# Kernel optimization log

Measured on AMD Instinct MI355X. Metric: run time of the kernel, lower is better.

The kernel has to match this reference:

```python
import jax, jax.numpy as jnp
import numpy as np

FP8 = jnp.float8_e4m3fn
FP8_MAX = 448.0  # float8_e4m3fn max finite value used by the module


def setup_inputs() -> dict:
    key = jax.random.key(0)
    k1, k2, k3 = jax.random.split(key, 3)
    x = jax.random.normal(k1, (4096, 4096), dtype=jnp.float32)          # [tokens, in_features]
    weight = jax.random.normal(k2, (16384, 4096), dtype=jnp.float32) * 0.02  # [out, in] fp32 master weight
    bias = jax.random.normal(k3, (16384,), dtype=jnp.float32) * 0.01
    return {"x": x, "weight": weight, "bias": bias}


def reference(x, weight, bias):
    # quantize_weight: per-tensor scale from fp32 weight, cast to fp8 (saturating)
    w_scale = FP8_MAX / (jnp.max(jnp.abs(weight)) + 1e-6)
    w_fp8 = (weight * w_scale).astype(FP8)
    # quantize_activation: per-tensor dynamic scale
    x_abs_max = jnp.max(jnp.abs(x)) + 1e-6
    x_scale = FP8_MAX / x_abs_max
    x_fp8 = (x * x_scale).astype(FP8)
    # upcast fp8 -> fp32 matmul, then descale + bias (same as torch module)
    out = jnp.matmul(x_fp8.astype(jnp.float32), w_fp8.astype(jnp.float32).T)
    out = out / (x_scale * w_scale)
    out = out + bias
    return out.astype(FP8)
```

## Files before the change

kernel.cpp:

```cpp
#include <hip/hip_runtime.h>
#include <math.h>
#include <stdint.h>

#define TOK  4096
#define KIN  4096
#define NOUT 16384

#define BM 128
#define BN 128
#define BK 64

#define FBM 64
#define FBN 64
#define FBK 32
#define FLDP (FBK + 2)

typedef int int32x4  __attribute__((ext_vector_type(4)));
typedef int int32x16 __attribute__((ext_vector_type(16)));

__global__ void init_ws_kernel(unsigned int* hdr) {
  if (threadIdx.x < 2) hdr[threadIdx.x] = 0u;
}

__global__ void absmax_kernel(const float4* __restrict__ src, int n4,
                              unsigned int* __restrict__ dst) {
  float m = 0.0f;
  for (int i = blockIdx.x * blockDim.x + threadIdx.x; i < n4;
       i += gridDim.x * blockDim.x) {
    float4 v = src[i];
    m = fmaxf(m, fmaxf(fmaxf(fabsf(v.x), fabsf(v.y)),
                       fmaxf(fabsf(v.z), fabsf(v.w))));
  }
#pragma unroll
  for (int off = 32; off > 0; off >>= 1) m = fmaxf(m, __shfl_down(m, off, 64));
  __shared__ float sm[4];
  if ((threadIdx.x & 63) == 0) sm[threadIdx.x >> 6] = m;
  __syncthreads();
  if (threadIdx.x == 0) {
    m = fmaxf(fmaxf(sm[0], sm[1]), fmaxf(sm[2], sm[3]));
    atomicMax(dst, __float_as_uint(m));
  }
}

__device__ __forceinline__ float scale_f32(unsigned int maxbits) {
  return __fdiv_rn(448.0f, __fadd_rn(__uint_as_float(maxbits), 1e-6f));
}

__device__ __forceinline__ unsigned char enc_fp8_f32(float v) {
  unsigned char s = (v < 0.0f) ? 0x80 : 0x00;
  float a = fabsf(v);
  if (a == 0.0f) return s;
  int e2;
  (void)frexpf(a, &e2);
  int p = e2 - 4;
  if (p < -9) p = -9;
  int n = (int)rintf(ldexpf(a, -p));
  if (n == 16) { n = 8; p += 1; }
  int E, mm;
  if (n >= 8) { E = p + 10; mm = n - 8; }
  else        { E = 0;      mm = n;     }
  return (unsigned char)(s | (E << 3) | mm);
}

__device__ __forceinline__ double out_value(double v) {
  if (v == 0.0) return 0.0;
  double a = fabs(v);
  int e2;
  (void)frexp(a, &e2);
  int p = e2 - 4;
  if (p < -9) p = -9;
  double t = ldexp(a, -p);
  double r;
  if (p <= -2) {
    r = ldexp(floor(t) + 0.5, p);
  } else {
    int n = (int)rint(t);
    if (n == 16) { n = 8; p += 1; }
    r = ldexp((double)n, p);
  }
  return (v < 0.0) ? -r : r;
}

__global__ void encode_kernel(const float* __restrict__ src, int n,
                              const unsigned int* __restrict__ maxbits,
                              unsigned char* __restrict__ codes) {
  const float scale = scale_f32(*maxbits);
  for (int i = blockIdx.x * blockDim.x + threadIdx.x; i < n;
       i += gridDim.x * blockDim.x) {
    codes[i] = enc_fp8_f32(__fmul_rn(src[i], scale));
  }
}

__global__ void encode_digits_kernel(const float4* __restrict__ src, int n4,
                                     const unsigned int* __restrict__ maxbits,
                                     unsigned int* __restrict__ p0,
                                     unsigned int* __restrict__ p1,
                                     unsigned int* __restrict__ p2) {
  const float scale = scale_f32(*maxbits);
  for (int i = blockIdx.x * blockDim.x + threadIdx.x; i < n4;
       i += gridDim.x * blockDim.x) {
    float4 v = src[i];
    const float f[4] = {v.x, v.y, v.z, v.w};
    unsigned int b0 = 0, b1 = 0, b2 = 0;
#pragma unroll
    for (int j = 0; j < 4; ++j) {
      unsigned char c = enc_fp8_f32(__fmul_rn(f[j], scale));
      int E = (c >> 3) & 15, mm = c & 7;
      int mag = E ? ((8 + mm) << (E - 1)) : mm;
      int iv = (c & 0x80) ? -mag : mag;
      int d0 = ((iv + 64) & 127) - 64;
      int t1 = (iv - d0) >> 7;
      int d1 = ((t1 + 64) & 127) - 64;
      int d2 = (t1 - d1) >> 7;
      b0 |= (unsigned int)(d0 & 255) << (8 * j);
      b1 |= (unsigned int)(d1 & 255) << (8 * j);
      b2 |= (unsigned int)(d2 & 255) << (8 * j);
    }
    p0[i] = b0; p1[i] = b1; p2[i] = b2;
  }
}

__device__ __forceinline__ void glds16(const void* g, void* l) {
  __builtin_amdgcn_global_load_lds(
      (const __attribute__((address_space(1))) void*)g,
      (__attribute__((address_space(3))) void*)l, 16, 0, 0);
}

__global__ __launch_bounds__(512, 2) void gemm_i8_kernel(
    const int8_t* __restrict__ xd, const int8_t* __restrict__ wd,
    const float* __restrict__ bias, const unsigned int* __restrict__ hdr,
    float* __restrict__ out) {
  constexpr int PLANE = BM * BK;
  constexpr int BUF   = 6 * PLANE;
  __shared__ __attribute__((aligned(16))) int8_t lds[2 * BUF];

  const int tid  = threadIdx.x;
  const int lane = tid & 63;
  const int wv   = tid >> 6;
  const int wm   = wv >> 1;
  const int wn   = wv & 1;

  const int swz = (blockIdx.x & 7) * ((int)gridDim.x >> 3) + ((int)blockIdx.x >> 3);
  const int n0 = (swz & (NOUT / BN - 1)) * BN;
  const int m0 = (swz / (NOUT / BN)) * BM;

  const int srow = lane >> 2;
  const int su   = (lane & 3) ^ ((lane >> 3) & 3);
  const int8_t* asrc = xd + (size_t)(m0 + wv * 16 + srow) * KIN + su * 16;
  const int8_t* bsrc = wd + (size_t)(n0 + wv * 16 + srow) * KIN + su * 16;
  const size_t XPL = (size_t)TOK * KIN;
  const size_t WPL = (size_t)NOUT * KIN;

  const int arow  = wm * 32 + (lane & 31);
  const int aoff  = arow * BK + ((((lane >> 5) ^ (arow >> 1)) & 3) << 4);
  const int brow0 = wn * 64 + (lane & 31);
  const int brow1 = brow0 + 32;
  const int boff0 = brow0 * BK + ((((lane >> 5) ^ (brow0 >> 1)) & 3) << 4);
  const int boff1 = brow1 * BK + ((((lane >> 5) ^ (brow1 >> 1)) & 3) << 4);

  int32x16 acc[2][5] = {};

  {
    int8_t* lb = lds + wv * 1024;
#pragma unroll
    for (int p = 0; p < 3; ++p) {
      glds16(asrc + p * XPL, lb + p * PLANE);
      glds16(bsrc + p * WPL, lb + (3 + p) * PLANE);
    }
  }
  __syncthreads();

  int cur = 0;
  for (int t = 0; t < KIN / BK; ++t) {
    if (t + 1 < KIN / BK) {
      int8_t* lb = lds + (cur ^ 1) * BUF + wv * 1024;
      const int k0 = (t + 1) * BK;
#pragma unroll
      for (int p = 0; p < 3; ++p) {
        glds16(asrc + p * XPL + k0, lb + p * PLANE);
        glds16(bsrc + p * WPL + k0, lb + (3 + p) * PLANE);
      }
    }
    const int8_t* lb = lds + cur * BUF;
#pragma unroll
    for (int kk = 0; kk < 2; ++kk) {
      const int kx = kk << 5;
      int32x4 af[3], bf0[3], bf1[3];
#pragma unroll
      for (int p = 0; p < 3; ++p) {
        af[p]  = *(const int32x4*)(lb + p * PLANE + (aoff ^ kx));
        bf0[p] = *(const int32x4*)(lb + (3 + p) * PLANE + (boff0 ^ kx));
        bf1[p] = *(const int32x4*)(lb + (3 + p) * PLANE + (boff1 ^ kx));
      }
#pragma unroll
      for (int pa = 0; pa < 3; ++pa)
#pragma unroll
        for (int pb = 0; pb < 3; ++pb) {
          acc[0][pa + pb] = __builtin_amdgcn_mfma_i32_32x32x32_i8(
              af[pa], bf0[pb], acc[0][pa + pb], 0, 0, 0);
          acc[1][pa + pb] = __builtin_amdgcn_mfma_i32_32x32x32_i8(
              af[pa], bf1[pb], acc[1][pa + pb], 0, 0, 0);
        }
    }
    __syncthreads();
    cur ^= 1;
  }

  const float xs  = scale_f32(hdr[0]);
  const float wsc = scale_f32(hdr[1]);
  const double denom = (double)__fmul_rn(xs, wsc);

#pragma unroll
  for (int s = 0; s < 2; ++s) {
    const int n = n0 + wn * 64 + s * 32 + (lane & 31);
    const double bn = (double)bias[n];
#pragma unroll
    for (int r = 0; r < 16; ++r) {
      const int m = m0 + wm * 32 + (r & 3) + 8 * (r >> 2) + 4 * (lane >> 5);
      double S = (double)acc[s][0][r]
               + 128.0       * (double)acc[s][1][r]
               + 16384.0     * (double)acc[s][2][r]
               + 2097152.0   * (double)acc[s][3][r]
               + 268435456.0 * (double)acc[s][4][r];
      double tt = S * 0x1p-18;
      tt = tt / denom;
      tt += bn;
      out[(size_t)m * NOUT + n] = (float)out_value(tt);
    }
  }
}

__global__ __launch_bounds__(256) void gemm_fp64_kernel(
    const uint8_t* __restrict__ xq, const uint8_t* __restrict__ wq,
    const float* __restrict__ bias, const unsigned int* __restrict__ hdr,
    float* __restrict__ out) {
  __shared__ double As[FBM][FLDP];
  __shared__ double Bs[FBN][FLDP];
  __shared__ float lut[256];

  const int tid = threadIdx.x;
  {
    int E = (tid >> 3) & 15, mm = tid & 7;
    float mag = E ? ldexpf((float)(8 + mm), E - 10) : ldexpf((float)mm, -9);
    lut[tid] = (tid & 0x80) ? -mag : mag;
  }
  const float xs  = scale_f32(hdr[0]);
  const float wsc = scale_f32(hdr[1]);
  const double denom = (double)__fmul_rn(xs, wsc);

  const int m0 = blockIdx.y * FBM;
  const int n0 = blockIdx.x * FBN;
  const int r  = tid >> 2;
  const int cb = (tid & 3) * 8;
  const int rt = tid >> 4;
  const int ct = tid & 15;

  double acc[4][4] = {{0.0}};
  const uint8_t* pa = xq + (size_t)(m0 + r) * KIN + cb;
  const uint8_t* pb = wq + (size_t)(n0 + r) * KIN + cb;

  __syncthreads();
  for (int k0 = 0; k0 < KIN; k0 += FBK) {
    uint2 ua = *(const uint2*)(pa + k0);
    uint2 ub = *(const uint2*)(pb + k0);
    unsigned wa0 = ua.x, wa1 = ua.y, wb0 = ub.x, wb1 = ub.y;
#pragma unroll
    for (int b = 0; b < 4; b++) {
      As[r][cb + b]     = (double)lut[(wa0 >> (8 * b)) & 255];
      As[r][cb + 4 + b] = (double)lut[(wa1 >> (8 * b)) & 255];
      Bs[r][cb + b]     = (double)lut[(wb0 >> (8 * b)) & 255];
      Bs[r][cb + 4 + b] = (double)lut[(wb1 >> (8 * b)) & 255];
    }
    __syncthreads();
#pragma unroll 8
    for (int kk = 0; kk < FBK; kk++) {
      double a[4], bb[4];
#pragma unroll
      for (int i = 0; i < 4; i++) a[i] = As[rt + 16 * i][kk];
#pragma unroll
      for (int j = 0; j < 4; j++) bb[j] = Bs[ct + 16 * j][kk];
#pragma unroll
      for (int i = 0; i < 4; i++)
#pragma unroll
        for (int j = 0; j < 4; j++)
          acc[i][j] = fma(a[i], bb[j], acc[i][j]);
    }
    __syncthreads();
  }

#pragma unroll
  for (int i = 0; i < 4; i++) {
    const int m = m0 + rt + 16 * i;
#pragma unroll
    for (int j = 0; j < 4; j++) {
      const int n = n0 + ct + 16 * j;
      double t = acc[i][j] / denom;
      t += (double)bias[n];
      out[(size_t)m * NOUT + n] = (float)out_value(t);
    }
  }
}

extern "C" void kernel_launch(void* const* d_in, const int* in_sizes, int n_in,
                              void* d_out, int out_size, void* d_ws,
                              size_t ws_size, hipStream_t stream) {
  const float* x    = (const float*)d_in[0];
  const float* w    = (const float*)d_in[1];
  const float* bias = (const float*)d_in[2];
  float* out        = (float*)d_out;

  unsigned int* hdr = (unsigned int*)d_ws;

  hipLaunchKernelGGL(init_ws_kernel, dim3(1), dim3(64), 0, stream, hdr);
  hipLaunchKernelGGL(absmax_kernel, dim3(1024), dim3(256), 0, stream,
                     (const float4*)x, TOK * KIN / 4, hdr + 0);
  hipLaunchKernelGGL(absmax_kernel, dim3(2048), dim3(256), 0, stream,
                     (const float4*)w, NOUT * KIN / 4, hdr + 1);

  const size_t TOKK = (size_t)TOK * KIN;
  const size_t NK   = (size_t)NOUT * KIN;
  const size_t need = 64 + 3 * TOKK + 3 * NK;

  if (ws_size >= need) {
    int8_t* xd = (int8_t*)d_ws + 64;
    int8_t* wd = xd + 3 * TOKK;
    hipLaunchKernelGGL(encode_digits_kernel, dim3(2048), dim3(256), 0, stream,
                       (const float4*)x, (int)(TOKK / 4), hdr + 0,
                       (unsigned int*)xd,
                       (unsigned int*)(xd + TOKK),
                       (unsigned int*)(xd + 2 * TOKK));
    hipLaunchKernelGGL(encode_digits_kernel, dim3(4096), dim3(256), 0, stream,
                       (const float4*)w, (int)(NK / 4), hdr + 1,
                       (unsigned int*)wd,
                       (unsigned int*)(wd + NK),
                       (unsigned int*)(wd + 2 * NK));
    hipLaunchKernelGGL(gemm_i8_kernel,
                       dim3((NOUT / BN) * (TOK / BM)), dim3(512), 0, stream,
                       xd, wd, bias, hdr, out);
  } else {
    uint8_t* xq = (uint8_t*)d_ws + 64;
    uint8_t* wq = xq + TOKK;
    hipLaunchKernelGGL(encode_kernel, dim3(2048), dim3(256), 0, stream, x,
                       TOK * KIN, hdr + 0, xq);
    hipLaunchKernelGGL(encode_kernel, dim3(4096), dim3(256), 0, stream, w,
                       NOUT * KIN, hdr + 1, wq);
    hipLaunchKernelGGL(gemm_fp64_kernel, dim3(NOUT / FBN, TOK / FBM),
                       dim3(256), 0, stream, xq, wq, bias, hdr, out);
  }
}
```

Baseline: 2.658 ms.

## Triple-buffer int8 GEMM K-loop with one barrier and XCD-aware tile mapping

```diff
diff --git a/kernel.cpp b/kernel.cpp
--- a/kernel.cpp
+++ b/kernel.cpp
@@ -9,6 +9,7 @@
 #define BM 128
 #define BN 128
 #define BK 64
+#define NT (KIN / BK)
 
 #define FBM 64
 #define FBN 64
@@ -132,7 +133,7 @@
     float* __restrict__ out) {
   constexpr int PLANE = BM * BK;
   constexpr int BUF   = 6 * PLANE;
-  __shared__ __attribute__((aligned(16))) int8_t lds[2 * BUF];
+  __shared__ __attribute__((aligned(16))) int8_t lds[3 * BUF];
 
   const int tid  = threadIdx.x;
   const int lane = tid & 63;
@@ -140,9 +141,11 @@
   const int wm   = wv >> 1;
   const int wn   = wv & 1;
 
-  const int swz = (blockIdx.x & 7) * ((int)gridDim.x >> 3) + ((int)blockIdx.x >> 3);
-  const int n0 = (swz & (NOUT / BN - 1)) * BN;
-  const int m0 = (swz / (NOUT / BN)) * BM;
+  const int bid = (int)blockIdx.x;
+  const int xcd = bid & 7;
+  const int c   = bid >> 3;
+  const int m0  = (c & 31) * BM;
+  const int n0  = ((xcd << 4) + (c >> 5)) * BN;
 
   const int srow = lane >> 2;
   const int su   = (lane & 3) ^ ((lane >> 3) & 3);
@@ -160,27 +163,28 @@
 
   int32x16 acc[2][5] = {};
 
-  {
-    int8_t* lb = lds + wv * 1024;
+  auto STAGE = [&](int buf, int t) {
+    int8_t* lb = lds + buf * BUF + wv * 1024;
+    const int k0 = t * BK;
 #pragma unroll
     for (int p = 0; p < 3; ++p) {
-      glds16(asrc + p * XPL, lb + p * PLANE);
-      glds16(bsrc + p * WPL, lb + (3 + p) * PLANE);
-    }
-  }
-  __syncthreads();
-
-  int cur = 0;
-  for (int t = 0; t < KIN / BK; ++t) {
-    if (t + 1 < KIN / BK) {
-      int8_t* lb = lds + (cur ^ 1) * BUF + wv * 1024;
-      const int k0 = (t + 1) * BK;
-#pragma unroll
-      for (int p = 0; p < 3; ++p) {
-        glds16(asrc + p * XPL + k0, lb + p * PLANE);
-        glds16(bsrc + p * WPL + k0, lb + (3 + p) * PLANE);
-      }
-    }
+      glds16(asrc + p * XPL + k0, lb + p * PLANE);
+      glds16(bsrc + p * WPL + k0, lb + (3 + p) * PLANE);
+    }
+  };
+
+  STAGE(0, 0);
+  STAGE(1, 1);
+
+  int cur = 0, stg = 2;
+  for (int t = 0; t < NT; ++t) {
+    if (t + 1 < NT) asm volatile("s_waitcnt vmcnt(6)" ::: "memory");
+    else            asm volatile("s_waitcnt vmcnt(0)" ::: "memory");
+    __builtin_amdgcn_s_barrier();
+    __builtin_amdgcn_sched_barrier(0);
+    if (t + 2 < NT) STAGE(stg, t + 2);
+    __builtin_amdgcn_sched_barrier(0);
+
     const int8_t* lb = lds + cur * BUF;
 #pragma unroll
     for (int kk = 0; kk < 2; ++kk) {
@@ -192,6 +196,7 @@
         bf0[p] = *(const int32x4*)(lb + (3 + p) * PLANE + (boff0 ^ kx));
         bf1[p] = *(const int32x4*)(lb + (3 + p) * PLANE + (boff1 ^ kx));
       }
+      __builtin_amdgcn_s_setprio(1);
 #pragma unroll
       for (int pa = 0; pa < 3; ++pa)
 #pragma unroll
@@ -201,9 +206,10 @@
           acc[1][pa + pb] = __builtin_amdgcn_mfma_i32_32x32x32_i8(
               af[pa], bf1[pb], acc[1][pa + pb], 0, 0, 0);
         }
-    }
-    __syncthreads();
-    cur ^= 1;
+      __builtin_amdgcn_s_setprio(0);
+    }
+    cur = (cur == 2) ? 0 : cur + 1;
+    stg = (stg == 2) ? 0 : stg + 1;
   }
 
   const float xs  = scale_f32(hdr[0]);
```

New measurement: 2.455 ms. 1.08x faster.
